# Performance work log

Hardware: AMD Instinct MI355X
Metric: run time of the kernel (lower is better)

## Reference

```python
import jax, jax.numpy as jnp
import numpy as np

P = 8        # patch size
STRIDE = 4   # reference patch stride
SR = 12      # search radius
SS = 3       # search step -> 9x9 = 81 candidates
K = 16       # group size (3rd dim of 3D transform)
LAM = 2.7    # hard threshold multiplier
TWO_STEP = True


def _dct_mat(n):
    k = np.arange(n)[:, None].astype(np.float64)
    i = np.arange(n)[None, :].astype(np.float64)
    m = np.cos(np.pi * (2 * i + 1) * k / (2 * n)) * np.sqrt(2.0 / n)
    m[0] /= np.sqrt(2.0)
    return jnp.asarray(m, jnp.float32)


def _hadamard(n):
    h = np.array([[1.0]])
    while h.shape[0] < n:
        h = np.kron(h, np.array([[1.0, 1.0], [1.0, -1.0]])) / np.sqrt(2.0)
    return jnp.asarray(h, jnp.float32)

D8 = _dct_mat(P)
H16 = _hadamard(K)


def _extract_patches(img):
    # img (H, W) -> (Hp*Wp, P*P) patches at stride 1
    H, W = img.shape
    Hp, Wp = H - P + 1, W - P + 1
    cols = [img[di:di + Hp, dj:dj + Wp] for di in range(P) for dj in range(P)]
    return jnp.stack(cols, -1).reshape(Hp * Wp, P * P), Hp, Wp


def _block_match(patches, Hp, Wp):
    # returns (N, K) flat patch indices of best-matching groups
    ri = jnp.arange(0, Hp, STRIDE)
    rj = jnp.arange(0, Wp, STRIDE)
    RI, RJ = jnp.meshgrid(ri, rj, indexing='ij')
    RI, RJ = RI.reshape(-1), RJ.reshape(-1)                     # (N,)
    offs = jnp.arange(-SR, SR + 1, SS)
    OI, OJ = jnp.meshgrid(offs, offs, indexing='ij')
    ci = jnp.clip(RI[:, None] + OI.reshape(-1)[None, :], 0, Hp - 1)
    cj = jnp.clip(RJ[:, None] + OJ.reshape(-1)[None, :], 0, Wp - 1)
    cidx = ci * Wp + cj                                         # (N, C)
    cand = patches[cidx]                                        # (N, C, 64)
    ref = patches[RI * Wp + RJ]                                 # (N, 64)
    dist = (jnp.sum(cand * cand, -1)
            - 2.0 * jnp.einsum('nce,ne->nc', cand, ref)
            + jnp.sum(ref * ref, -1)[:, None])
    _, top = jax.lax.top_k(-dist, K)
    return jnp.take_along_axis(cidx, top, axis=1)               # (N, K)


def _fwd3d(groups):
    # (N, K, P*P) -> 3D transform coeffs (N, K, P, P)
    g = groups.reshape(groups.shape[0], K, P, P)
    c = jnp.einsum('ab,nkbc,dc->nkad', D8, g, D8)   # 2D DCT per patch
    return jnp.einsum('gk,nkad->ngad', H16, c)      # 1D Hadamard across group


def _inv3d(coef):
    c = jnp.einsum('gk,ngad->nkad', H16, coef)      # H^T (orthonormal)
    g = jnp.einsum('ab,nkad,dc->nkbc', D8, c, D8)   # inverse 2D DCT
    return g.reshape(coef.shape[0], K, P * P)


def _aggregate(vals, w, gidx, Hp, Wp, H, W):
    # vals (N,K,64) filtered patches, w (N,) group weights, gidx (N,K)
    gi, gj = gidx // Wp, gidx % Wp
    offs = (jnp.arange(P)[:, None] * W + jnp.arange(P)[None, :]).reshape(-1)
    pix = ((gi * W + gj)[..., None] + offs).reshape(-1)         # (N*K*64,)
    wv = jnp.broadcast_to(w[:, None, None], vals.shape)
    num = jnp.zeros(H * W, jnp.float32).at[pix].add((wv * vals).reshape(-1))
    den = jnp.zeros(H * W, jnp.float32).at[pix].add(wv.reshape(-1))
    return (num / jnp.maximum(den, 1e-8)).reshape(H, W)


def _bm3d_channel(img, sigma2):
    H, W = img.shape
    sigma2 = jnp.float32(sigma2)
    sigma = jnp.sqrt(sigma2)
    patches, Hp, Wp = _extract_patches(img)

    # ---- step 1: hard-threshold collaborative filtering ----
    gidx = _block_match(patches, Hp, Wp)
    groups = patches[gidx]                                      # (N,K,64)
    coef = _fwd3d(groups)
    mask = (jnp.abs(coef) > LAM * sigma)
    mask = mask.at[:, 0, 0, 0].set(True)                        # keep DC
    coef_ht = jnp.where(mask, coef, 0.0)
    nnz = jnp.sum(mask.astype(jnp.float32), axis=(1, 2, 3))
    w_ht = 1.0 / (sigma2 * jnp.maximum(nnz, 1.0))
    basic = _aggregate(_inv3d(coef_ht), w_ht, gidx, Hp, Wp, H, W)
    if not TWO_STEP:
        return basic

    # ---- step 2: Wiener filtering using the basic estimate ----
    patches_b, _, _ = _extract_patches(basic)
    gidx2 = _block_match(patches_b, Hp, Wp)
    cb = _fwd3d(patches_b[gidx2])                               # basic coeffs
    cn = _fwd3d(patches[gidx2])                                 # noisy coeffs
    wien = cb * cb / (cb * cb + sigma2)
    coef_w = wien * cn
    w_wie = 1.0 / (sigma2 * jnp.maximum(jnp.sum(wien * wien, axis=(1, 2, 3)), 1e-8))
    return _aggregate(_inv3d(coef_w), w_wie, gidx2, Hp, Wp, H, W)


def setup_inputs() -> dict:
    key = jax.random.key(0)
    im = jax.random.randint(key, (1, 1, 384, 384), 0, 256, dtype=jnp.int32)
    return {"im": im, "variance": 25}


def reference(im, variance):
    # im: (1, 1, H, W) int tensor, values >= 0; variance: scalar noise variance
    outs = [_bm3d_channel(im[0, c].astype(jnp.float32), variance)
            for c in range(im.shape[1])]
    return jnp.stack(outs, 0)[None]                             # (1, C, H, W) float32
```

## Files before the change

### kernel.cpp

```cpp
#include <hip/hip_runtime.h>
#include <math.h>

#define TS 48
#define FINF 3.4e38f

__device__ __forceinline__ int iclip(int v, int hi) {
  return v < 0 ? 0 : (v > hi ? hi : v);
}

constexpr float CA = 0.35355339059327373f;
constexpr float K1 = 0.49039264020161522f;
constexpr float K2 = 0.46193976625564337f;
constexpr float K3 = 0.41573480615127262f;
constexpr float K4 = 0.35355339059327379f;
constexpr float K5 = 0.27778511650980111f;
constexpr float K6 = 0.19134171618254489f;
constexpr float K7 = 0.097545161008064135f;

constexpr float DCT8[8][8] = {
  { CA, CA, CA, CA, CA, CA, CA, CA},
  { K1, K3, K5, K7,-K7,-K5,-K3,-K1},
  { K2, K6,-K6,-K2,-K2,-K6, K6, K2},
  { K3,-K7,-K1,-K5, K5, K1, K7,-K3},
  { K4,-K4,-K4, K4, K4,-K4,-K4, K4},
  { K5,-K1, K7, K3,-K3,-K7, K1,-K5},
  { K6,-K2, K2,-K6,-K6, K2,-K2, K6},
  { K7,-K5, K3,-K1, K1,-K3, K5,-K7},
};

__device__ __forceinline__ int sxor_i(int v, int m) {
  switch (m) {
    case 1:  return __builtin_amdgcn_update_dpp(0, v, 0xB1, 0xF, 0xF, true);
    case 2:  return __builtin_amdgcn_update_dpp(0, v, 0x4E, 0xF, 0xF, true);
    case 4:  return __builtin_amdgcn_ds_swizzle(v, (4 << 10) | 0x1F);
    case 8:  return __builtin_amdgcn_update_dpp(0, v, 0x128, 0xF, 0xF, true);
    case 16: return __builtin_amdgcn_ds_swizzle(v, (16 << 10) | 0x1F);
    default: return __shfl_xor(v, 32, 64);
  }
}
__device__ __forceinline__ float sxor_f(float v, int m) {
  return __int_as_float(sxor_i(__float_as_int(v), m));
}

__device__ __forceinline__ float qbcast(float v, int s) {
  int x = __float_as_int(v), r;
  switch (s) {
    case 0:  r = __builtin_amdgcn_update_dpp(0, x, 0x00, 0xF, 0xF, true); break;
    case 1:  r = __builtin_amdgcn_update_dpp(0, x, 0x55, 0xF, 0xF, true); break;
    case 2:  r = __builtin_amdgcn_update_dpp(0, x, 0xAA, 0xF, 0xF, true); break;
    default: r = __builtin_amdgcn_update_dpp(0, x, 0xFF, 0xF, 0xF, true); break;
  }
  return __int_as_float(r);
}

__device__ __forceinline__ void fwd_rowcol(float X[2][8], float U[2][8],
                                           const float Ca0[8], const float Ca1[8]) {
#pragma unroll
  for (int r = 0; r < 2; r++)
#pragma unroll
    for (int d = 0; d < 8; d++) {
      float s = X[r][0] * DCT8[d][0];
#pragma unroll
      for (int c = 1; c < 8; c++) s += X[r][c] * DCT8[d][c];
      U[r][d] = s;
    }
#pragma unroll
  for (int r = 0; r < 2; r++)
#pragma unroll
    for (int d = 0; d < 8; d++) X[r][d] = 0.f;
#pragma unroll
  for (int b = 0; b < 8; b++)
#pragma unroll
    for (int d = 0; d < 8; d++) {
      float yb = qbcast(U[b & 1][d], b >> 1);
      X[0][d] += Ca0[b] * yb;
      X[1][d] += Ca1[b] * yb;
    }
}

__device__ __forceinline__ void inv_colrow(float X[2][8], float U[2][8],
                                           const float Ct0[8], const float Ct1[8]) {
#pragma unroll
  for (int r = 0; r < 2; r++)
#pragma unroll
    for (int d = 0; d < 8; d++) U[r][d] = 0.f;
#pragma unroll
  for (int a = 0; a < 8; a++)
#pragma unroll
    for (int d = 0; d < 8; d++) {
      float za = qbcast(X[a & 1][d], a >> 1);
      U[0][d] += Ct0[a] * za;
      U[1][d] += Ct1[a] * za;
    }
#pragma unroll
  for (int r = 0; r < 2; r++)
#pragma unroll
    for (int c = 0; c < 8; c++) {
      float s = U[r][0] * DCT8[0][c];
#pragma unroll
      for (int d = 1; d < 8; d++) s += U[r][d] * DCT8[d][c];
      X[r][c] = s;
    }
}

__device__ __forceinline__ void had16r(float X[2][8], int lane) {
#pragma unroll
  for (int m = 4; m <= 32; m <<= 1) {
    bool hi = (lane & m) != 0;
#pragma unroll
    for (int r = 0; r < 2; r++)
#pragma unroll
      for (int d = 0; d < 8; d++) {
        float tv = sxor_f(X[r][d], m);
        X[r][d] = hi ? (tv - X[r][d]) : (X[r][d] + tv);
      }
  }
#pragma unroll
  for (int r = 0; r < 2; r++)
#pragma unroll
    for (int d = 0; d < 8; d++) X[r][d] *= 0.25f;
}

template <int WIEN>
__global__ __launch_bounds__(256, 4) void bm3d_pass(
    const int* __restrict__ img, const float* __restrict__ basic,
    const int* __restrict__ pvar,
    float* __restrict__ num, float* __restrict__ den) {
  __shared__ float ldsD[64], ldsDT[64];
  __shared__ __align__(16) float wdist[4][84];
  __shared__ int wsel[4][16];
  __shared__ float Rws[32 * 40];
  __shared__ float S2[25 * 40];
  __shared__ float bufA[32 * TS];
  __shared__ float bufB[32 * TS];

  int t = threadIdx.x;
  int brow = blockIdx.x / 24, bcb = blockIdx.x - brow * 24;
  int ri = brow * 4;
  int bim = ri - 12;       int bi = bim < 0 ? 0 : (bim > 352 ? 352 : bim);
  int ubm = 16 * bcb - 12; int ub = ubm < 0 ? 0 : (ubm > 352 ? 352 : ubm);

  if (t < 64) ldsD[t] = DCT8[t >> 3][t & 7];
  else if (t < 128) { int u = t - 64; ldsDT[u] = DCT8[u & 7][u >> 3]; }

  for (int e4 = t; e4 < 352; e4 += 256) {
    int r = e4 / 11, c4 = (e4 - r * 11) << 2;
    int col = ub + c4;
    int gidx = (bi + r) * 384 + col;
    int o = r * TS + c4;
    if (col + 3 < 384) {
      int4 iv = *(const int4*)&img[gidx];
      float4 fv = make_float4((float)iv.x, (float)iv.y, (float)iv.z, (float)iv.w);
      if (WIEN) {
        *(float4*)&bufA[o] = *(const float4*)&basic[gidx];
        *(float4*)&bufB[o] = fv;
      } else {
        *(float4*)&bufA[o] = fv;
      }
    } else {
#pragma unroll
      for (int u = 0; u < 4; u++) {
        bool ok = (col + u) < 384;
        float fi = ok ? (float)img[gidx + u] : 0.f;
        if (WIEN) {
          bufA[o + u] = ok ? basic[gidx + u] : 0.f;
          bufB[o + u] = fi;
        } else {
          bufA[o + u] = fi;
        }
      }
    }
  }
  __syncthreads();

  for (int e = t; e < 32 * 37; e += 256) {
    int r = e / 37, j = e - r * 37;
    const float* p = bufA + r * TS + j;
    float s = 0.f;
#pragma unroll
    for (int d = 0; d < 8; d++) { float v = p[d]; s += v * v; }
    Rws[r * 40 + j] = s;
  }
  __syncthreads();
  for (int e = t; e < 25 * 37; e += 256) {
    int i = e / 37, j = e - i * 37;
    float s = 0.f;
#pragma unroll
    for (int d = 0; d < 8; d++) s += Rws[(i + d) * 40 + j];
    S2[i * 40 + j] = s;
  }
  __syncthreads();

  float sigma2 = (float)pvar[0];
  int wv = t >> 6, lane = t & 63;
  int gc = bcb * 4 + wv;
  bool active = gc < 95;
  int rj = (active ? gc : 94) * 4;

  const float* tileS = bufA;
  const float* tileN = WIEN ? bufB : bufA;

  int cB = lane < 17 ? 64 + lane : 80;
  int aiA = iclip(ri + (lane / 9) * 3 - 12, 376) - bi;
  int ajA = iclip(rj + (lane % 9) * 3 - 12, 376) - ub;
  int aiB = iclip(ri + (cB / 9) * 3 - 12, 376) - bi;
  int ajB = iclip(rj + (cB % 9) * 3 - 12, 376) - ub;
  int roi = ri - bi, roj = rj - ub;

  float scrA = 0.f, scrB = 0.f;
#pragma unroll
  for (int i = 0; i < 8; i++) {
    float4 ra = *(const float4*)(tileS + (roi + i) * TS + roj);
    float4 rb = *(const float4*)(tileS + (roi + i) * TS + roj + 4);
    float rv[8] = {ra.x, ra.y, ra.z, ra.w, rb.x, rb.y, rb.z, rb.w};
    const float* ap = tileS + (aiA + i) * TS + ajA;
    const float* bp = tileS + (aiB + i) * TS + ajB;
#pragma unroll
    for (int j = 0; j < 8; j++) {
      scrA += ap[j] * rv[j];
      scrB += bp[j] * rv[j];
    }
  }
  float srr = S2[roi * 40 + roj];
  float dA = fmaf(-2.f, scrA, S2[aiA * 40 + ajA]) + srr;
  float dB = lane < 17 ? fmaf(-2.f, scrB, S2[aiB * 40 + ajB]) + srr : FINF;

  wdist[wv][lane] = dA;
  if (lane < 17)      wdist[wv][64 + lane] = dB;
  else if (lane < 20) wdist[wv][64 + lane] = FINF;

  int rA = 0, rB = 0;
  const float4* wp = (const float4*)&wdist[wv][0];
  int idxB = 64 + lane;
#pragma unroll 3
  for (int c4 = 0; c4 < 21; c4++) {
    float4 v = wp[c4];
    float ev[4] = {v.x, v.y, v.z, v.w};
#pragma unroll
    for (int u = 0; u < 4; u++) {
      int c2 = c4 * 4 + u;
      rA += (ev[u] < dA || (ev[u] == dA && c2 < lane)) ? 1 : 0;
      rB += (ev[u] < dB || (ev[u] == dB && c2 < idxB)) ? 1 : 0;
    }
  }
  if (rA < 16) wsel[wv][rA] = (aiA << 8) | ajA;
  if (lane < 17 && rB < 16) wsel[wv][rB] = (aiB << 8) | ajB;

  int k = lane >> 2, q = lane & 3;
  int sp = wsel[wv][k];
  int gi0 = (sp >> 8) + 2 * q, gj0 = sp & 255;

  float Ca0[8], Ca1[8];
  *(float4*)&Ca0[0] = *(const float4*)&ldsD[(2 * q) * 8];
  *(float4*)&Ca0[4] = *(const float4*)&ldsD[(2 * q) * 8 + 4];
  *(float4*)&Ca1[0] = *(const float4*)&ldsD[(2 * q + 1) * 8];
  *(float4*)&Ca1[4] = *(const float4*)&ldsD[(2 * q + 1) * 8 + 4];

  float X[2][8], U[2][8];
  float w;

  if (WIEN) {
    float Z[2][8];
#pragma unroll
    for (int r = 0; r < 2; r++)
#pragma unroll
      for (int c = 0; c < 8; c++) Z[r][c] = tileS[(gi0 + r) * TS + gj0 + c];
    fwd_rowcol(Z, U, Ca0, Ca1);
    had16r(Z, lane);

#pragma unroll
    for (int r = 0; r < 2; r++)
#pragma unroll
      for (int c = 0; c < 8; c++) X[r][c] = tileN[(gi0 + r) * TS + gj0 + c];
    fwd_rowcol(X, U, Ca0, Ca1);
    had16r(X, lane);

    float p = 0.f;
#pragma unroll
    for (int r = 0; r < 2; r++)
#pragma unroll
      for (int d = 0; d < 8; d++) {
        float cb = Z[r][d];
        float we = cb * cb / (cb * cb + sigma2);
        X[r][d] = we * X[r][d];
        p += we * we;
      }
#pragma unroll
    for (int m = 1; m <= 32; m <<= 1) p += sxor_f(p, m);
    w = 1.f / (sigma2 * fmaxf(p, 1e-8f));
  } else {
#pragma unroll
    for (int r = 0; r < 2; r++)
#pragma unroll
      for (int c = 0; c < 8; c++) X[r][c] = tileN[(gi0 + r) * TS + gj0 + c];
    fwd_rowcol(X, U, Ca0, Ca1);
    had16r(X, lane);

    float thr = 2.7f * sqrtf(sigma2);
    int cnt = 0;
#pragma unroll
    for (int r = 0; r < 2; r++)
#pragma unroll
      for (int d = 0; d < 8; d++) {
        bool keep = (fabsf(X[r][d]) > thr) || (lane == 0 && r == 0 && d == 0);
        cnt += (int)__popcll(__ballot(keep));
        if (!keep) X[r][d] = 0.f;
      }
    w = 1.f / (sigma2 * fmaxf((float)cnt, 1.f));
  }

  had16r(X, lane);
#pragma unroll
  for (int a = 0; a < 8; a++) {
    Ca0[a] = ldsDT[(2 * q) * 8 + a];
    Ca1[a] = ldsDT[(2 * q + 1) * 8 + a];
  }
  inv_colrow(X, U, Ca0, Ca1);

  __syncthreads();
  for (int e = t; e < 32 * TS; e += 256) { bufA[e] = 0.f; bufB[e] = 0.f; }
  __syncthreads();

  if (active) {
#pragma unroll
    for (int r = 0; r < 2; r++)
#pragma unroll
      for (int c = 0; c < 8; c++) {
        int off = (gi0 + r) * TS + gj0 + c;
        atomicAdd(&bufA[off], w * X[r][c]);
        atomicAdd(&bufB[off], w);
      }
  }
  __syncthreads();

  for (int e = t; e < 32 * TS; e += 256) {
    float dv = bufB[e];
    if (dv != 0.f) {
      int r = e / TS, c = e - r * TS;
      int gp = (bi + r) * 384 + ub + c;
      atomicAdd(&num[gp], bufA[e]);
      atomicAdd(&den[gp], dv);
    }
  }
}

__global__ void div_kernel(const float* __restrict__ num,
                           const float* __restrict__ den,
                           float* __restrict__ out, int npix) {
  int i = blockIdx.x * blockDim.x + threadIdx.x;
  if (i < npix) out[i] = num[i] / fmaxf(den[i], 1e-8f);
}

extern "C" void kernel_launch(void* const* d_in, const int* in_sizes, int n_in,
                              void* d_out, int out_size, void* d_ws, size_t ws_size,
                              hipStream_t stream) {
  const int* img  = (const int*)d_in[0];
  const int* pvar = (const int*)d_in[1];
  float* out = (float*)d_out;
  float* ws  = (float*)d_ws;

  const int NPIX = 384 * 384;
  float* num1  = ws + 0 * NPIX;
  float* den1  = ws + 1 * NPIX;
  float* basic = ws + 2 * NPIX;
  float* num2  = ws + 3 * NPIX;
  float* den2  = ws + 4 * NPIX;

  hipMemsetAsync(num1, 0, (size_t)2 * NPIX * sizeof(float), stream);
  hipMemsetAsync(num2, 0, (size_t)2 * NPIX * sizeof(float), stream);

  const int NBLK = 95 * 24;
  bm3d_pass<0><<<NBLK, 256, 0, stream>>>(img, nullptr, pvar, num1, den1);
  div_kernel<<<(NPIX + 255) / 256, 256, 0, stream>>>(num1, den1, basic, NPIX);
  bm3d_pass<1><<<NBLK, 256, 0, stream>>>(img, basic, pvar, num2, den2);
  div_kernel<<<(NPIX + 255) / 256, 256, 0, stream>>>(num2, den2, out, NPIX);
}
```

Before: 314.2 us.

## Process 4x4 reference patches per block with a shared 44x44 tile

Each block now covers a 4x4 grid of reference patches (16 rows by 16 columns of image) instead of a single row of four. It loads one 44x44 tile, computes the patch-energy table once for it, and loops each wave over four reference rows, accumulating aggregation results in LDS before flushing to global atomics once. This removes the redundant overlapping tile loads, the repeated energy sums and the global atomic traffic that came from 95x24 small blocks. In exchange there are far fewer blocks (576), more LDS per block and serial work per wave, which may hurt occupancy and latency hiding.

```diff
diff --git a/kernel.cpp b/kernel.cpp
--- a/kernel.cpp
+++ b/kernel.cpp
@@ -1,7 +1,8 @@
 #include <hip/hip_runtime.h>
 #include <math.h>
 
-#define TS 48
+#define TW 44
+#define SW 40
 #define FINF 3.4e38f
 
 __device__ __forceinline__ int iclip(int v, int hi) {
@@ -129,216 +130,203 @@
   __shared__ float ldsD[64], ldsDT[64];
   __shared__ __align__(16) float wdist[4][84];
   __shared__ int wsel[4][16];
-  __shared__ float Rws[32 * 40];
-  __shared__ float S2[25 * 40];
-  __shared__ float bufA[32 * TS];
-  __shared__ float bufB[32 * TS];
+  __shared__ float S2[37 * SW];
+  __shared__ float tileS[44 * TW];
+  __shared__ float tileN[WIEN ? 44 * TW : 1];
+  __shared__ float accN[44 * TW];
+  __shared__ float accD[44 * TW];
 
   int t = threadIdx.x;
-  int brow = blockIdx.x / 24, bcb = blockIdx.x - brow * 24;
-  int ri = brow * 4;
-  int bim = ri - 12;       int bi = bim < 0 ? 0 : (bim > 352 ? 352 : bim);
-  int ubm = 16 * bcb - 12; int ub = ubm < 0 ? 0 : (ubm > 352 ? 352 : ubm);
+  int brow = blockIdx.x / 24, bcol = blockIdx.x - brow * 24;
+  int bi0 = brow * 16 - 12; int bi = bi0 < 0 ? 0 : (bi0 > 340 ? 340 : bi0);
+  int ub0 = bcol * 16 - 12; int ub = ub0 < 0 ? 0 : (ub0 > 340 ? 340 : ub0);
 
   if (t < 64) ldsD[t] = DCT8[t >> 3][t & 7];
   else if (t < 128) { int u = t - 64; ldsDT[u] = DCT8[u & 7][u >> 3]; }
 
-  for (int e4 = t; e4 < 352; e4 += 256) {
+  for (int e4 = t; e4 < 484; e4 += 256) {
     int r = e4 / 11, c4 = (e4 - r * 11) << 2;
-    int col = ub + c4;
-    int gidx = (bi + r) * 384 + col;
-    int o = r * TS + c4;
-    if (col + 3 < 384) {
-      int4 iv = *(const int4*)&img[gidx];
-      float4 fv = make_float4((float)iv.x, (float)iv.y, (float)iv.z, (float)iv.w);
-      if (WIEN) {
-        *(float4*)&bufA[o] = *(const float4*)&basic[gidx];
-        *(float4*)&bufB[o] = fv;
-      } else {
-        *(float4*)&bufA[o] = fv;
-      }
+    int gidx = (bi + r) * 384 + ub + c4;
+    int o = r * TW + c4;
+    int4 iv = *(const int4*)&img[gidx];
+    float4 fv = make_float4((float)iv.x, (float)iv.y, (float)iv.z, (float)iv.w);
+    if (WIEN) {
+      *(float4*)&tileS[o] = *(const float4*)&basic[gidx];
+      *(float4*)&tileN[o] = fv;
     } else {
-#pragma unroll
-      for (int u = 0; u < 4; u++) {
-        bool ok = (col + u) < 384;
-        float fi = ok ? (float)img[gidx + u] : 0.f;
-        if (WIEN) {
-          bufA[o + u] = ok ? basic[gidx + u] : 0.f;
-          bufB[o + u] = fi;
-        } else {
-          bufA[o + u] = fi;
-        }
-      }
-    }
-  }
-  __syncthreads();
-
-  for (int e = t; e < 32 * 37; e += 256) {
+      *(float4*)&tileS[o] = fv;
+    }
+  }
+  __syncthreads();
+
+  float* Rws = accN;
+  for (int e = t; e < 44 * 37; e += 256) {
     int r = e / 37, j = e - r * 37;
-    const float* p = bufA + r * TS + j;
+    const float* p = tileS + r * TW + j;
     float s = 0.f;
 #pragma unroll
     for (int d = 0; d < 8; d++) { float v = p[d]; s += v * v; }
-    Rws[r * 40 + j] = s;
-  }
-  __syncthreads();
-  for (int e = t; e < 25 * 37; e += 256) {
+    Rws[r * SW + j] = s;
+  }
+  __syncthreads();
+  for (int e = t; e < 37 * 37; e += 256) {
     int i = e / 37, j = e - i * 37;
     float s = 0.f;
 #pragma unroll
-    for (int d = 0; d < 8; d++) s += Rws[(i + d) * 40 + j];
-    S2[i * 40 + j] = s;
-  }
+    for (int d = 0; d < 8; d++) s += Rws[(i + d) * SW + j];
+    S2[i * SW + j] = s;
+  }
+  __syncthreads();
+  for (int e = t; e < 44 * TW; e += 256) { accN[e] = 0.f; accD[e] = 0.f; }
   __syncthreads();
 
   float sigma2 = (float)pvar[0];
   int wv = t >> 6, lane = t & 63;
-  int gc = bcb * 4 + wv;
-  bool active = gc < 95;
-  int rj = (active ? gc : 94) * 4;
-
-  const float* tileS = bufA;
-  const float* tileN = WIEN ? bufB : bufA;
-
+  int rc = bcol * 4 + wv;
+  bool colAct = rc < 95;
+  int rj = (colAct ? rc : 94) * 4;
+  int roj = rj - ub;
   int cB = lane < 17 ? 64 + lane : 80;
-  int aiA = iclip(ri + (lane / 9) * 3 - 12, 376) - bi;
   int ajA = iclip(rj + (lane % 9) * 3 - 12, 376) - ub;
-  int aiB = iclip(ri + (cB / 9) * 3 - 12, 376) - bi;
   int ajB = iclip(rj + (cB % 9) * 3 - 12, 376) - ub;
-  int roi = ri - bi, roj = rj - ub;
-
-  float scrA = 0.f, scrB = 0.f;
-#pragma unroll
-  for (int i = 0; i < 8; i++) {
-    float4 ra = *(const float4*)(tileS + (roi + i) * TS + roj);
-    float4 rb = *(const float4*)(tileS + (roi + i) * TS + roj + 4);
-    float rv[8] = {ra.x, ra.y, ra.z, ra.w, rb.x, rb.y, rb.z, rb.w};
-    const float* ap = tileS + (aiA + i) * TS + ajA;
-    const float* bp = tileS + (aiB + i) * TS + ajB;
-#pragma unroll
-    for (int j = 0; j < 8; j++) {
-      scrA += ap[j] * rv[j];
-      scrB += bp[j] * rv[j];
-    }
-  }
-  float srr = S2[roi * 40 + roj];
-  float dA = fmaf(-2.f, scrA, S2[aiA * 40 + ajA]) + srr;
-  float dB = lane < 17 ? fmaf(-2.f, scrB, S2[aiB * 40 + ajB]) + srr : FINF;
-
-  wdist[wv][lane] = dA;
-  if (lane < 17)      wdist[wv][64 + lane] = dB;
-  else if (lane < 20) wdist[wv][64 + lane] = FINF;
-
-  int rA = 0, rB = 0;
-  const float4* wp = (const float4*)&wdist[wv][0];
-  int idxB = 64 + lane;
+  int k = lane >> 2, q = lane & 3;
+  const float* tileNN = WIEN ? tileN : tileS;
+
+  for (int it = 0; it < 4; it++) {
+    int rr = brow * 4 + it;
+    if (!(colAct && rr < 95)) continue;
+    int ri = rr * 4;
+    int roi = ri - bi;
+    int aiA = iclip(ri + (lane / 9) * 3 - 12, 376) - bi;
+    int aiB = iclip(ri + (cB / 9) * 3 - 12, 376) - bi;
+
+    float scrA = 0.f, scrB = 0.f;
+#pragma unroll
+    for (int i = 0; i < 8; i++) {
+      float4 ra = *(const float4*)(tileS + (roi + i) * TW + roj);
+      float4 rb = *(const float4*)(tileS + (roi + i) * TW + roj + 4);
+      float rv[8] = {ra.x, ra.y, ra.z, ra.w, rb.x, rb.y, rb.z, rb.w};
+      const float* ap = tileS + (aiA + i) * TW + ajA;
+      const float* bp = tileS + (aiB + i) * TW + ajB;
+#pragma unroll
+      for (int j = 0; j < 8; j++) {
+        scrA += ap[j] * rv[j];
+        scrB += bp[j] * rv[j];
+      }
+    }
+    float srr = S2[roi * SW + roj];
+    float dA = fmaf(-2.f, scrA, S2[aiA * SW + ajA]) + srr;
+    float dB = lane < 17 ? fmaf(-2.f, scrB, S2[aiB * SW + ajB]) + srr : FINF;
+
+    wdist[wv][lane] = dA;
+    if (lane < 17)      wdist[wv][64 + lane] = dB;
+    else if (lane < 20) wdist[wv][64 + lane] = FINF;
+
+    int rA = 0, rB = 0;
+    const float4* wp = (const float4*)&wdist[wv][0];
+    int idxB = 64 + lane;
 #pragma unroll 3
-  for (int c4 = 0; c4 < 21; c4++) {
-    float4 v = wp[c4];
-    float ev[4] = {v.x, v.y, v.z, v.w};
-#pragma unroll
-    for (int u = 0; u < 4; u++) {
-      int c2 = c4 * 4 + u;
-      rA += (ev[u] < dA || (ev[u] == dA && c2 < lane)) ? 1 : 0;
-      rB += (ev[u] < dB || (ev[u] == dB && c2 < idxB)) ? 1 : 0;
-    }
-  }
-  if (rA < 16) wsel[wv][rA] = (aiA << 8) | ajA;
-  if (lane < 17 && rB < 16) wsel[wv][rB] = (aiB << 8) | ajB;
-
-  int k = lane >> 2, q = lane & 3;
-  int sp = wsel[wv][k];
-  int gi0 = (sp >> 8) + 2 * q, gj0 = sp & 255;
-
-  float Ca0[8], Ca1[8];
-  *(float4*)&Ca0[0] = *(const float4*)&ldsD[(2 * q) * 8];
-  *(float4*)&Ca0[4] = *(const float4*)&ldsD[(2 * q) * 8 + 4];
-  *(float4*)&Ca1[0] = *(const float4*)&ldsD[(2 * q + 1) * 8];
-  *(float4*)&Ca1[4] = *(const float4*)&ldsD[(2 * q + 1) * 8 + 4];
-
-  float X[2][8], U[2][8];
-  float w;
-
-  if (WIEN) {
-    float Z[2][8];
+    for (int c4 = 0; c4 < 21; c4++) {
+      float4 v = wp[c4];
+      float ev[4] = {v.x, v.y, v.z, v.w};
+#pragma unroll
+      for (int u = 0; u < 4; u++) {
+        int c2 = c4 * 4 + u;
+        rA += (ev[u] < dA || (ev[u] == dA && c2 < lane)) ? 1 : 0;
+        rB += (ev[u] < dB || (ev[u] == dB && c2 < idxB)) ? 1 : 0;
+      }
+    }
+    if (rA < 16) wsel[wv][rA] = (aiA << 8) | ajA;
+    if (lane < 17 && rB < 16) wsel[wv][rB] = (aiB << 8) | ajB;
+
+    int sp = wsel[wv][k];
+    int gi0 = (sp >> 8) + 2 * q, gj0 = sp & 255;
+
+    float Ca0[8], Ca1[8];
+    *(float4*)&Ca0[0] = *(const float4*)&ldsD[(2 * q) * 8];
+    *(float4*)&Ca0[4] = *(const float4*)&ldsD[(2 * q) * 8 + 4];
+    *(float4*)&Ca1[0] = *(const float4*)&ldsD[(2 * q + 1) * 8];
+    *(float4*)&Ca1[4] = *(const float4*)&ldsD[(2 * q + 1) * 8 + 4];
+
+    float X[2][8], U[2][8];
+    float w;
+
+    if (WIEN) {
+      float Z[2][8];
+#pragma unroll
+      for (int r = 0; r < 2; r++)
+#pragma unroll
+        for (int c = 0; c < 8; c++) Z[r][c] = tileS[(gi0 + r) * TW + gj0 + c];
+      fwd_rowcol(Z, U, Ca0, Ca1);
+      had16r(Z, lane);
+
+#pragma unroll
+      for (int r = 0; r < 2; r++)
+#pragma unroll
+        for (int c = 0; c < 8; c++) X[r][c] = tileNN[(gi0 + r) * TW + gj0 + c];
+      fwd_rowcol(X, U, Ca0, Ca1);
+      had16r(X, lane);
+
+      float p = 0.f;
+#pragma unroll
+      for (int r = 0; r < 2; r++)
+#pragma unroll
+        for (int d = 0; d < 8; d++) {
+          float cb = Z[r][d];
+          float we = cb * cb / (cb * cb + sigma2);
+          X[r][d] = we * X[r][d];
+          p += we * we;
+        }
+#pragma unroll
+      for (int m = 1; m <= 32; m <<= 1) p += sxor_f(p, m);
+      w = 1.f / (sigma2 * fmaxf(p, 1e-8f));
+    } else {
+#pragma unroll
+      for (int r = 0; r < 2; r++)
+#pragma unroll
+        for (int c = 0; c < 8; c++) X[r][c] = tileNN[(gi0 + r) * TW + gj0 + c];
+      fwd_rowcol(X, U, Ca0, Ca1);
+      had16r(X, lane);
+
+      float thr = 2.7f * sqrtf(sigma2);
+      int cnt = 0;
+#pragma unroll
+      for (int r = 0; r < 2; r++)
+#pragma unroll
+        for (int d = 0; d < 8; d++) {
+          bool keep = (fabsf(X[r][d]) > thr) || (lane == 0 && r == 0 && d == 0);
+          cnt += (int)__popcll(__ballot(keep));
+          if (!keep) X[r][d] = 0.f;
+        }
+      w = 1.f / (sigma2 * fmaxf((float)cnt, 1.f));
+    }
+
+    had16r(X, lane);
+    float Ct0[8], Ct1[8];
+#pragma unroll
+    for (int a = 0; a < 8; a++) {
+      Ct0[a] = ldsDT[(2 * q) * 8 + a];
+      Ct1[a] = ldsDT[(2 * q + 1) * 8 + a];
+    }
+    inv_colrow(X, U, Ct0, Ct1);
+
 #pragma unroll
     for (int r = 0; r < 2; r++)
 #pragma unroll
-      for (int c = 0; c < 8; c++) Z[r][c] = tileS[(gi0 + r) * TS + gj0 + c];
-    fwd_rowcol(Z, U, Ca0, Ca1);
-    had16r(Z, lane);
-
-#pragma unroll
-    for (int r = 0; r < 2; r++)
-#pragma unroll
-      for (int c = 0; c < 8; c++) X[r][c] = tileN[(gi0 + r) * TS + gj0 + c];
-    fwd_rowcol(X, U, Ca0, Ca1);
-    had16r(X, lane);
-
-    float p = 0.f;
-#pragma unroll
-    for (int r = 0; r < 2; r++)
-#pragma unroll
-      for (int d = 0; d < 8; d++) {
-        float cb = Z[r][d];
-        float we = cb * cb / (cb * cb + sigma2);
-        X[r][d] = we * X[r][d];
-        p += we * we;
+      for (int c = 0; c < 8; c++) {
+        int off = (gi0 + r) * TW + gj0 + c;
+        atomicAdd(&accN[off], w * X[r][c]);
+        atomicAdd(&accD[off], w);
       }
-#pragma unroll
-    for (int m = 1; m <= 32; m <<= 1) p += sxor_f(p, m);
-    w = 1.f / (sigma2 * fmaxf(p, 1e-8f));
-  } else {
-#pragma unroll
-    for (int r = 0; r < 2; r++)
-#pragma unroll
-      for (int c = 0; c < 8; c++) X[r][c] = tileN[(gi0 + r) * TS + gj0 + c];
-    fwd_rowcol(X, U, Ca0, Ca1);
-    had16r(X, lane);
-
-    float thr = 2.7f * sqrtf(sigma2);
-    int cnt = 0;
-#pragma unroll
-    for (int r = 0; r < 2; r++)
-#pragma unroll
-      for (int d = 0; d < 8; d++) {
-        bool keep = (fabsf(X[r][d]) > thr) || (lane == 0 && r == 0 && d == 0);
-        cnt += (int)__popcll(__ballot(keep));
-        if (!keep) X[r][d] = 0.f;
-      }
-    w = 1.f / (sigma2 * fmaxf((float)cnt, 1.f));
-  }
-
-  had16r(X, lane);
-#pragma unroll
-  for (int a = 0; a < 8; a++) {
-    Ca0[a] = ldsDT[(2 * q) * 8 + a];
-    Ca1[a] = ldsDT[(2 * q + 1) * 8 + a];
-  }
-  inv_colrow(X, U, Ca0, Ca1);
-
-  __syncthreads();
-  for (int e = t; e < 32 * TS; e += 256) { bufA[e] = 0.f; bufB[e] = 0.f; }
-  __syncthreads();
-
-  if (active) {
-#pragma unroll
-    for (int r = 0; r < 2; r++)
-#pragma unroll
-      for (int c = 0; c < 8; c++) {
-        int off = (gi0 + r) * TS + gj0 + c;
-        atomicAdd(&bufA[off], w * X[r][c]);
-        atomicAdd(&bufB[off], w);
-      }
-  }
-  __syncthreads();
-
-  for (int e = t; e < 32 * TS; e += 256) {
-    float dv = bufB[e];
+  }
+
+  __syncthreads();
+  for (int e = t; e < 44 * TW; e += 256) {
+    float dv = accD[e];
     if (dv != 0.f) {
-      int r = e / TS, c = e - r * TS;
+      int r = e / TW, c = e - r * TW;
       int gp = (bi + r) * 384 + ub + c;
-      atomicAdd(&num[gp], bufA[e]);
+      atomicAdd(&num[gp], accN[e]);
       atomicAdd(&den[gp], dv);
     }
   }
@@ -369,7 +357,7 @@
   hipMemsetAsync(num1, 0, (size_t)2 * NPIX * sizeof(float), stream);
   hipMemsetAsync(num2, 0, (size_t)2 * NPIX * sizeof(float), stream);
 
-  const int NBLK = 95 * 24;
+  const int NBLK = 24 * 24;
   bm3d_pass<0><<<NBLK, 256, 0, stream>>>(img, nullptr, pvar, num1, den1);
   div_kernel<<<(NPIX + 255) / 256, 256, 0, stream>>>(num1, den1, basic, NPIX);
   bm3d_pass<1><<<NBLK, 256, 0, stream>>>(img, basic, pvar, num2, den2);
```

New measurement: 391.7 us. 24.7% more time.
